# Performance work log

Measured on AMD Instinct MI355X. Metric: run time of the kernel, lower is better.

The kernel has to match this reference:

```python
import jax, jax.numpy as jnp
import numpy as np
import math

B, S, H, DK = 16, 4096, 16, 64
DM = H * DK          # 1024, d_model
QD = 1024            # q_d_model
KVD = 1024           # kv_d_model
MASK_P = 0.85        # randbool probability


def setup_inputs() -> dict:
    key = jax.random.key(0)
    ks = jax.random.split(key, 12)
    s = 0.02
    return {
        "q": jax.random.normal(ks[0], (B, 1, QD), jnp.float32),
        "k": jax.random.normal(ks[1], (B, S, KVD), jnp.float32),
        "v": jax.random.normal(ks[2], (B, S, KVD), jnp.float32),
        "Wq": jax.random.normal(ks[3], (QD, DM), jnp.float32) * s,
        "bq": jnp.zeros((DM,), jnp.float32),
        "Wk": jax.random.normal(ks[4], (KVD, DM), jnp.float32) * s,
        "bk": jnp.zeros((DM,), jnp.float32),
        "Wv": jax.random.normal(ks[5], (KVD, DM), jnp.float32) * s,
        "bv": jnp.zeros((DM,), jnp.float32),
        "Wo": jax.random.normal(ks[6], (DM, QD), jnp.float32) * s,
        "bo": jnp.zeros((QD,), jnp.float32),
        # randbool(shape, p=0.85): True where rand < p -> score zeroed
        "maskfill": jax.random.uniform(ks[7], (B, H, 1, S)) < MASK_P,
    }


def reference(q, k, v, Wq, bq, Wk, bk, Wv, bv, Wo, bo, maskfill):
    bs = q.shape[0]
    # projections -> [B, L, H, DK] -> [B, H, L, DK]
    qh = (q @ Wq + bq).reshape(bs, -1, H, DK).transpose(0, 2, 1, 3)  # [B,H,1,DK]
    kh = (k @ Wk + bk).reshape(bs, -1, H, DK).transpose(0, 2, 1, 3)  # [B,H,S,DK]
    vh = (v @ Wv + bv).reshape(bs, -1, H, DK).transpose(0, 2, 1, 3)  # [B,H,S,DK]

    scores1 = jnp.einsum("bhqd,bhkd->bhqk", qh, kh) / math.sqrt(DK)  # [B,H,1,S]

    # plain path (dropout = identity in eval)
    attn = jax.nn.softmax(scores1, axis=-1)
    out_h = jnp.einsum("bhqk,bhkd->bhqd", attn, vh)                  # [B,H,1,DK]

    # masked path: zero-fill (not -inf) masked raw scores, then softmax
    masked_scores = jnp.where(maskfill, 0.0, scores1)
    mattn = jax.nn.softmax(masked_scores, axis=-1)
    mout_h = jnp.einsum("bhqk,bhkd->bhqd", mattn, vh)

    concat = out_h.transpose(0, 2, 1, 3).reshape(bs, DM)
    mconcat = mout_h.transpose(0, 2, 1, 3).reshape(bs, DM)
    output = concat @ Wo + bo
    masked_output = mconcat @ Wo + bo
    return (output, masked_output)
```

## Files before the change

kernel.cpp:

```cpp
#include <hip/hip_runtime.h>
#include <stdint.h>

#define NB 16
#define NS 4096
#define NH 16
#define NC 1024

#define OFF_QHP   0u
#define OFF_QK    262144u
#define OFF_QB    524288u
#define OFF_SP    524608u
#define OFF_CTXP  532800u
#define OFF_CON   8921408u

__global__ __launch_bounds__(128) void k_qh(
    const float* __restrict__ q, const float* __restrict__ Wq, float* __restrict__ qhp)
{
    __shared__ float qs[64*16];
    int dz = blockIdx.x, cs = blockIdx.y;
    int tid = threadIdx.x;
    int d = dz*128 + tid;
#pragma unroll
    for (int j = 0; j < 2; ++j) {
        int idx = j*128 + tid;
        int b = idx >> 4, c4 = (idx & 15) << 2;
        float4 t = *(const float4*)(q + (size_t)b*NC + cs*64 + c4);
        qs[(c4+0)*16 + b] = t.x; qs[(c4+1)*16 + b] = t.y;
        qs[(c4+2)*16 + b] = t.z; qs[(c4+3)*16 + b] = t.w;
    }
    __syncthreads();
    float acc[16];
#pragma unroll
    for (int b = 0; b < 16; ++b) acc[b] = 0.f;
#pragma unroll 4
    for (int c = 0; c < 64; ++c) {
        float w = Wq[(size_t)(cs*64 + c)*NC + d];
        const float4* qr = (const float4*)(qs + c*16);
        float4 q0 = qr[0], q1 = qr[1], q2 = qr[2], q3 = qr[3];
        acc[0]  = fmaf(w, q0.x, acc[0]);  acc[1]  = fmaf(w, q0.y, acc[1]);
        acc[2]  = fmaf(w, q0.z, acc[2]);  acc[3]  = fmaf(w, q0.w, acc[3]);
        acc[4]  = fmaf(w, q1.x, acc[4]);  acc[5]  = fmaf(w, q1.y, acc[5]);
        acc[6]  = fmaf(w, q1.z, acc[6]);  acc[7]  = fmaf(w, q1.w, acc[7]);
        acc[8]  = fmaf(w, q2.x, acc[8]);  acc[9]  = fmaf(w, q2.y, acc[9]);
        acc[10] = fmaf(w, q2.z, acc[10]); acc[11] = fmaf(w, q2.w, acc[11]);
        acc[12] = fmaf(w, q3.x, acc[12]); acc[13] = fmaf(w, q3.y, acc[13]);
        acc[14] = fmaf(w, q3.z, acc[14]); acc[15] = fmaf(w, q3.w, acc[15]);
    }
#pragma unroll
    for (int b = 0; b < 16; ++b) qhp[((size_t)cs*16 + b)*NC + d] = acc[b];
}

__global__ __launch_bounds__(128) void k_qk(
    const float* __restrict__ qhp, const float* __restrict__ bq,
    const float* __restrict__ Wk, const float* __restrict__ bk,
    float* __restrict__ qko, float* __restrict__ qbv)
{
    int h = blockIdx.x;
    int c = blockIdx.y*128 + threadIdx.x;
    __shared__ float qs[16*64];
    for (int j = 0; j < 8; ++j) {
        int idx = j*128 + threadIdx.x;
        int b = idx >> 6, dd = idx & 63;
        float a = bq[h*64 + dd];
#pragma unroll
        for (int cs = 0; cs < 16; ++cs) a += qhp[((size_t)cs*16 + b)*NC + h*64 + dd];
        qs[idx] = a;
    }
    __syncthreads();
    const float* wr = Wk + (size_t)c*NC + h*64;
    float acc[16];
#pragma unroll
    for (int b = 0; b < 16; ++b) acc[b] = 0.f;
#pragma unroll 4
    for (int d = 0; d < 64; ++d) {
        float w = wr[d];
#pragma unroll
        for (int b = 0; b < 16; ++b) acc[b] = fmaf(qs[b*64 + d], w, acc[b]);
    }
#pragma unroll
    for (int b = 0; b < 16; ++b) qko[((size_t)b*NH + h)*NC + c] = acc[b];
    if (blockIdx.y == 0 && threadIdx.x < 16) {
        int b = threadIdx.x; float a = 0.f;
        for (int d = 0; d < 64; ++d) a = fmaf(qs[b*64 + d], bk[h*64 + d], a);
        qbv[b*NH + h] = a;
    }
}

#define QTS 20
#define SCOMP(BUF, W)                                                          \
    _Pragma("unroll")                                                          \
    for (int j = 0; j < 4; ++j) {                                              \
        const float* qp = qt + ((W)*16 + ph*4 + j)*QTS + hg*4;                 \
        float4 qv = *(const float4*)qp;                                        \
        _Pragma("unroll")                                                      \
        for (int i = 0; i < 4; ++i) {                                          \
            float kc = (j == 0) ? BUF[i].x : (j == 1) ? BUF[i].y               \
                     : (j == 2) ? BUF[i].z : BUF[i].w;                         \
            acc[i][0] = fmaf(kc, qv.x, acc[i][0]);                             \
            acc[i][1] = fmaf(kc, qv.y, acc[i][1]);                             \
            acc[i][2] = fmaf(kc, qv.z, acc[i][2]);                             \
            acc[i][3] = fmaf(kc, qv.w, acc[i][3]);                             \
        }                                                                      \
    }
__global__ __launch_bounds__(1024) void k_att(
    const float* __restrict__ kk, const float* __restrict__ vv,
    const float* __restrict__ qkm, const float* __restrict__ qbv,
    const void* __restrict__ mask, float* __restrict__ ctxp, float* __restrict__ Sp)
{
    __shared__ float qt[512*QTS];
    __shared__ float attl[256*32];
    __shared__ float red[16][2][16];
    int sb = blockIdx.x, b = blockIdx.y;
    int tid = threadIdx.x;
    int ph = tid & 3, hg = (tid >> 2) & 3, rg = tid >> 4;
    int srow = sb*256 + rg*4;

    int fl;
    {
        const uint4* mw = (const uint4*)mask;
        unsigned f = 0u, g = 0u;
#pragma unroll
        for (int j = 0; j < 8; ++j) {
            uint4 m4 = mw[j];
            f |= (m4.x == 0x3F800000u) | (m4.y == 0x3F800000u)
               | (m4.z == 0x3F800000u) | (m4.w == 0x3F800000u);
            g |= ((m4.x > 1u) & (m4.x != 0x3F800000u))
               | ((m4.y > 1u) & (m4.y != 0x3F800000u))
               | ((m4.z > 1u) & (m4.z != 0x3F800000u))
               | ((m4.w > 1u) & (m4.w != 0x3F800000u));
        }
        fl = f ? 2 : (g ? 1 : 0);
    }

    const float* kr = kk + ((size_t)b*NS + srow)*NC + ph*4;
    float acc[4][4];
#pragma unroll
    for (int i = 0; i < 4; ++i)
#pragma unroll
        for (int j = 0; j < 4; ++j) acc[i][j] = 0.f;

    for (int cz = 0; cz < 2; ++cz) {
        __syncthreads();
#pragma unroll
        for (int j = 0; j < 8; ++j) {
            int idx = j*1024 + tid;
            int h = idx >> 9, c = idx & 511;
            qt[c*QTS + h] = qkm[((size_t)b*NH + h)*NC + cz*512 + c];
        }
        __syncthreads();
        const float* kc0 = kr + cz*512;
        float4 A[4], B[4], T[4];
#pragma unroll
        for (int i = 0; i < 4; ++i) A[i] = *(const float4*)(kc0 + i*NC);
#pragma unroll
        for (int i = 0; i < 4; ++i) B[i] = *(const float4*)(kc0 + i*NC + 16);
        for (int w = 0; w < 32; w += 2) {
            if (w + 2 < 32) {
#pragma unroll
                for (int i = 0; i < 4; ++i)
                    T[i] = *(const float4*)(kc0 + i*NC + (w+2)*16);
            }
            SCOMP(A, w);
            if (w + 3 < 32) {
#pragma unroll
                for (int i = 0; i < 4; ++i)
                    A[i] = *(const float4*)(kc0 + i*NC + (w+3)*16);
            }
            SCOMP(B, (w+1));
#pragma unroll
            for (int i = 0; i < 4; ++i) { B[i] = A[i]; A[i] = T[i]; }
        }
    }
#pragma unroll
    for (int i = 0; i < 4; ++i)
#pragma unroll
        for (int j = 0; j < 4; ++j) {
            acc[i][j] += __shfl_xor(acc[i][j], 1, 64);
            acc[i][j] += __shfl_xor(acc[i][j], 2, 64);
        }
    float d0[4];
    if (ph == 0) {
#pragma unroll
        for (int j = 0; j < 4; ++j) d0[j] = acc[0][j];
    } else if (ph == 1) {
#pragma unroll
        for (int j = 0; j < 4; ++j) d0[j] = acc[1][j];
    } else if (ph == 2) {
#pragma unroll
        for (int j = 0; j < 4; ++j) d0[j] = acc[2][j];
    } else {
#pragma unroll
        for (int j = 0; j < 4; ++j) d0[j] = acc[3][j];
    }
    int lA = rg*4 + ph;
    int sA = sb*256 + lA;
    unsigned mA = 0;
    if (fl == 1) {
        const uint8_t* mp = (const uint8_t*)mask + (size_t)(b*NH + hg*4)*NS;
#pragma unroll
        for (int j = 0; j < 4; ++j)
            if (mp[(size_t)j*NS + sA]) mA |= (1u << j);
    } else if (fl == 2) {
        const float* mp = (const float*)mask + (size_t)(b*NH + hg*4)*NS;
#pragma unroll
        for (int j = 0; j < 4; ++j)
            if (mp[(size_t)j*NS + sA] != 0.f) mA |= (1u << j);
    } else {
        const int* mp = (const int*)mask + (size_t)(b*NH + hg*4)*NS;
#pragma unroll
        for (int j = 0; j < 4; ++j)
            if (mp[(size_t)j*NS + sA]) mA |= (1u << j);
    }
    float p0a[4], p1a[4], r0[4], r1[4];
#pragma unroll
    for (int j = 0; j < 4; ++j) {
        float qb = qbv[b*NH + hg*4 + j];
        float va = (d0[j] + qb) * 0.125f;
        p0a[j] = __expf(va);
        p1a[j] = (mA >> j & 1u) ? 1.0f : p0a[j];
        r0[j] = p0a[j];
        r1[j] = p1a[j];
    }
    {
        int swA = (lA & 7) << 2;
        *(float4*)(attl + lA*32 + ((hg*4) ^ swA))      = make_float4(p0a[0], p0a[1], p0a[2], p0a[3]);
        *(float4*)(attl + lA*32 + ((16 + hg*4) ^ swA)) = make_float4(p1a[0], p1a[1], p1a[2], p1a[3]);
    }
#pragma unroll
    for (int j = 0; j < 4; ++j) {
        r0[j] += __shfl_xor(r0[j], 1, 64);  r1[j] += __shfl_xor(r1[j], 1, 64);
        r0[j] += __shfl_xor(r0[j], 2, 64);  r1[j] += __shfl_xor(r1[j], 2, 64);
        r0[j] += __shfl_xor(r0[j], 16, 64); r1[j] += __shfl_xor(r1[j], 16, 64);
        r0[j] += __shfl_xor(r0[j], 32, 64); r1[j] += __shfl_xor(r1[j], 32, 64);
    }
    int wv = tid >> 6;
    if ((tid & 51) == 0) {
#pragma unroll
        for (int j = 0; j < 4; ++j) {
            red[wv][0][hg*4 + j] = r0[j];
            red[wv][1][hg*4 + j] = r1[j];
        }
    }
    __syncthreads();
    if (tid < 32) {
        int pa = tid >> 4, h = tid & 15;
        float a = 0.f;
#pragma unroll
        for (int w16 = 0; w16 < 16; ++w16) a += red[w16][pa][h];
        Sp[((size_t)b*16 + sb)*32 + tid] = a;
    }

    int cq = tid & 255, grp = tid >> 8;
    int p = grp >> 1, hh = grp & 1;
    float cacc[8][4];
#pragma unroll
    for (int u = 0; u < 8; ++u)
#pragma unroll
        for (int j = 0; j < 4; ++j) cacc[u][j] = 0.f;
    const float* vb = vv + ((size_t)b*NS + sb*256)*NC + cq*4;
    float4 vr[8], vn[8];
#pragma unroll
    for (int i = 0; i < 8; ++i) vr[i] = *(const float4*)(vb + (size_t)i*NC);
    int G0 = p*4 + hh*2;
    for (int r0q = 0; r0q < 256; r0q += 8) {
        if (r0q + 8 < 256) {
#pragma unroll
            for (int i = 0; i < 8; ++i)
                vn[i] = *(const float4*)(vb + (size_t)(r0q + 8 + i)*NC);
        }
#pragma unroll
        for (int i = 0; i < 8; ++i) {
            int r = r0q + i;
            const float* ar = attl + r*32;
            int lw = r & 7;
            float4 vcur = vr[i];
#pragma unroll
            for (int g2 = 0; g2 < 2; ++g2) {
                float4 aw = *(const float4*)(ar + (((G0 + g2) ^ lw) << 2));
                cacc[g2*4+0][0] = fmaf(aw.x, vcur.x, cacc[g2*4+0][0]);
                cacc[g2*4+0][1] = fmaf(aw.x, vcur.y, cacc[g2*4+0][1]);
                cacc[g2*4+0][2] = fmaf(aw.x, vcur.z, cacc[g2*4+0][2]);
                cacc[g2*4+0][3] = fmaf(aw.x, vcur.w, cacc[g2*4+0][3]);
                cacc[g2*4+1][0] = fmaf(aw.y, vcur.x, cacc[g2*4+1][0]);
                cacc[g2*4+1][1] = fmaf(aw.y, vcur.y, cacc[g2*4+1][1]);
                cacc[g2*4+1][2] = fmaf(aw.y, vcur.z, cacc[g2*4+1][2]);
                cacc[g2*4+1][3] = fmaf(aw.y, vcur.w, cacc[g2*4+1][3]);
                cacc[g2*4+2][0] = fmaf(aw.z, vcur.x, cacc[g2*4+2][0]);
                cacc[g2*4+2][1] = fmaf(aw.z, vcur.y, cacc[g2*4+2][1]);
                cacc[g2*4+2][2] = fmaf(aw.z, vcur.z, cacc[g2*4+2][2]);
                cacc[g2*4+2][3] = fmaf(aw.z, vcur.w, cacc[g2*4+2][3]);
                cacc[g2*4+3][0] = fmaf(aw.w, vcur.x, cacc[g2*4+3][0]);
                cacc[g2*4+3][1] = fmaf(aw.w, vcur.y, cacc[g2*4+3][1]);
                cacc[g2*4+3][2] = fmaf(aw.w, vcur.z, cacc[g2*4+3][2]);
                cacc[g2*4+3][3] = fmaf(aw.w, vcur.w, cacc[g2*4+3][3]);
            }
        }
#pragma unroll
        for (int i = 0; i < 8; ++i) vr[i] = vn[i];
    }
#pragma unroll
    for (int gh = 0; gh < 8; ++gh) {
        int head = hh*8 + gh;
        *(float4*)(ctxp + ((((size_t)sb*2 + p)*NB + b)*NH + head)*NC + cq*4)
            = make_float4(cacc[gh][0], cacc[gh][1], cacc[gh][2], cacc[gh][3]);
    }
}

__global__ __launch_bounds__(256) void k_outhN(
    const float* __restrict__ ctxp, const float* __restrict__ Sp,
    const float* __restrict__ Wv, const float* __restrict__ bv,
    float* __restrict__ con)
{
    int b = blockIdx.y, p = blockIdx.z;
    int dx = blockIdx.x;
    int d = dx*256 + threadIdx.x;
    int h0 = dx*4;
    __shared__ float cl[4*NC];
    float Sinv[4];
#pragma unroll
    for (int j = 0; j < 4; ++j) {
        float a = 0.f;
        for (int sb = 0; sb < 16; ++sb)
            a += Sp[((size_t)b*16 + sb)*32 + p*16 + h0 + j];
        Sinv[j] = 1.f / a;
    }
#pragma unroll
    for (int hh = 0; hh < 4; ++hh) {
        for (int cc = threadIdx.x; cc < NC; cc += 256) {
            float a = 0.f;
#pragma unroll
            for (int ss = 0; ss < 16; ++ss)
                a += ctxp[((((size_t)ss*2 + p)*NB + b)*NH + h0 + hh)*NC + cc];
            cl[hh*NC + cc] = a * Sinv[hh];
        }
    }
    __syncthreads();
    const float* c2 = cl + ((threadIdx.x >> 6) << 10);
    float a0=0.f,a1=0.f,a2=0.f,a3=0.f;
    for (int c = 0; c < NC; c += 4) {
        a0 = fmaf(c2[c+0], Wv[(size_t)(c+0)*NC + d], a0);
        a1 = fmaf(c2[c+1], Wv[(size_t)(c+1)*NC + d], a1);
        a2 = fmaf(c2[c+2], Wv[(size_t)(c+2)*NC + d], a2);
        a3 = fmaf(c2[c+3], Wv[(size_t)(c+3)*NC + d], a3);
    }
    con[((size_t)p*NB + b)*NC + d] = (a0+a1)+(a2+a3) + bv[d];
}

__global__ __launch_bounds__(256) void k_out(
    const float* __restrict__ con, const float* __restrict__ Wo,
    const float* __restrict__ bo, float* __restrict__ out)
{
    int b = blockIdx.y, p = blockIdx.z;
    int o = blockIdx.x*256 + threadIdx.x;
    __shared__ float cl[NC];
    for (int i = threadIdx.x; i < NC; i += 256)
        cl[i] = con[((size_t)p*NB + b)*NC + i];
    __syncthreads();
    float a0=0.f,a1=0.f,a2=0.f,a3=0.f;
    for (int m = 0; m < NC; m += 4) {
        a0 = fmaf(cl[m+0], Wo[(size_t)(m+0)*NC + o], a0);
        a1 = fmaf(cl[m+1], Wo[(size_t)(m+1)*NC + o], a1);
        a2 = fmaf(cl[m+2], Wo[(size_t)(m+2)*NC + o], a2);
        a3 = fmaf(cl[m+3], Wo[(size_t)(m+3)*NC + o], a3);
    }
    out[(size_t)p*NB*NC + (size_t)b*NC + o] = (a0+a1)+(a2+a3) + bo[o];
}

extern "C" void kernel_launch(void* const* d_in, const int* in_sizes, int n_in,
                              void* d_out, int out_size, void* d_ws, size_t ws_size,
                              hipStream_t stream)
{
    (void)in_sizes; (void)n_in; (void)out_size; (void)ws_size;
    const float* q  = (const float*)d_in[0];
    const float* k  = (const float*)d_in[1];
    const float* v  = (const float*)d_in[2];
    const float* Wq = (const float*)d_in[3];
    const float* bq = (const float*)d_in[4];
    const float* Wk = (const float*)d_in[5];
    const float* bk = (const float*)d_in[6];
    const float* Wv = (const float*)d_in[7];
    const float* bv = (const float*)d_in[8];
    const float* Wo = (const float*)d_in[9];
    const float* bo = (const float*)d_in[10];
    const void*  mk = d_in[11];

    float* ws   = (float*)d_ws;
    float* qhp  = ws + OFF_QHP;
    float* qkv  = ws + OFF_QK;
    float* qbv  = ws + OFF_QB;
    float* Sp   = ws + OFF_SP;
    float* ctxp = ws + OFF_CTXP;
    float* con  = ws + OFF_CON;
    float* out  = (float*)d_out;

    k_qh<<<dim3(8, 16), 128, 0, stream>>>(q, Wq, qhp);
    k_qk<<<dim3(16, 8), 128, 0, stream>>>(qhp, bq, Wk, bk, qkv, qbv);
    k_att<<<dim3(16, 16), 1024, 0, stream>>>(k, v, qkv, qbv, mk, ctxp, Sp);
    k_outhN<<<dim3(4, NB, 2), 256, 0, stream>>>(ctxp, Sp, Wv, bv, con);
    k_out<<<dim3(4, NB, 2), 256, 0, stream>>>(con, Wo, bo, out);
}
```

Measured before the change: 305.2 us.

## Split fused attention kernel into separate scores and context kernels

```diff
diff --git a/kernel.cpp b/kernel.cpp
--- a/kernel.cpp
+++ b/kernel.cpp
@@ -9,9 +9,10 @@
 #define OFF_QHP   0u
 #define OFF_QK    262144u
 #define OFF_QB    524288u
-#define OFF_SP    524608u
-#define OFF_CTXP  532800u
-#define OFF_CON   8921408u
+#define OFF_SP    524544u
+#define OFF_ATT   540928u
+#define OFF_CTXP  2638080u
+#define OFF_CON   11026688u
 
 __global__ __launch_bounds__(128) void k_qh(
     const float* __restrict__ q, const float* __restrict__ Wq, float* __restrict__ qhp)
@@ -87,7 +88,7 @@
 }
 
 #define QTS 20
-#define SCOMP(BUF, W)                                                          \
+#define SCOMP4(BUF, W)                                                         \
     _Pragma("unroll")                                                          \
     for (int j = 0; j < 4; ++j) {                                              \
         const float* qp = qt + ((W)*16 + ph*4 + j)*QTS + hg*4;                 \
@@ -102,18 +103,17 @@
             acc[i][3] = fmaf(kc, qv.w, acc[i][3]);                             \
         }                                                                      \
     }
-__global__ __launch_bounds__(1024) void k_att(
-    const float* __restrict__ kk, const float* __restrict__ vv,
-    const float* __restrict__ qkm, const float* __restrict__ qbv,
-    const void* __restrict__ mask, float* __restrict__ ctxp, float* __restrict__ Sp)
-{
-    __shared__ float qt[512*QTS];
-    __shared__ float attl[256*32];
-    __shared__ float red[16][2][16];
+__global__ __launch_bounds__(512, 4) void k_scoresS(
+    const float* __restrict__ kk, const float* __restrict__ qkm,
+    const float* __restrict__ qbv, const void* __restrict__ mask,
+    float* __restrict__ att, float* __restrict__ Sp)
+{
+    __shared__ float qt[256*QTS];
+    __shared__ float red[8][2][16];
     int sb = blockIdx.x, b = blockIdx.y;
     int tid = threadIdx.x;
     int ph = tid & 3, hg = (tid >> 2) & 3, rg = tid >> 4;
-    int srow = sb*256 + rg*4;
+    int srow = sb*128 + rg*4;
 
     int fl;
     {
@@ -139,36 +139,28 @@
 #pragma unroll
         for (int j = 0; j < 4; ++j) acc[i][j] = 0.f;
 
-    for (int cz = 0; cz < 2; ++cz) {
+    for (int cz = 0; cz < 4; ++cz) {
         __syncthreads();
 #pragma unroll
         for (int j = 0; j < 8; ++j) {
-            int idx = j*1024 + tid;
-            int h = idx >> 9, c = idx & 511;
-            qt[c*QTS + h] = qkm[((size_t)b*NH + h)*NC + cz*512 + c];
+            int idx = j*512 + tid;
+            int h = idx >> 8, c = idx & 255;
+            qt[c*QTS + h] = qkm[((size_t)b*NH + h)*NC + cz*256 + c];
         }
         __syncthreads();
-        const float* kc0 = kr + cz*512;
-        float4 A[4], B[4], T[4];
+        const float* kc0 = kr + cz*256;
+        float4 A[4], B[4];
 #pragma unroll
         for (int i = 0; i < 4; ++i) A[i] = *(const float4*)(kc0 + i*NC);
-#pragma unroll
-        for (int i = 0; i < 4; ++i) B[i] = *(const float4*)(kc0 + i*NC + 16);
-        for (int w = 0; w < 32; w += 2) {
-            if (w + 2 < 32) {
+        for (int w = 0; w < 16; ++w) {
+            if (w < 15) {
 #pragma unroll
                 for (int i = 0; i < 4; ++i)
-                    T[i] = *(const float4*)(kc0 + i*NC + (w+2)*16);
+                    B[i] = *(const float4*)(kc0 + i*NC + (w+1)*16);
             }
-            SCOMP(A, w);
-            if (w + 3 < 32) {
-#pragma unroll
-                for (int i = 0; i < 4; ++i)
-                    A[i] = *(const float4*)(kc0 + i*NC + (w+3)*16);
-            }
-            SCOMP(B, (w+1));
-#pragma unroll
-            for (int i = 0; i < 4; ++i) { B[i] = A[i]; A[i] = T[i]; }
+            SCOMP4(A, w);
+#pragma unroll
+            for (int i = 0; i < 4; ++i) A[i] = B[i];
         }
     }
 #pragma unroll
@@ -193,7 +185,7 @@
         for (int j = 0; j < 4; ++j) d0[j] = acc[3][j];
     }
     int lA = rg*4 + ph;
-    int sA = sb*256 + lA;
+    int sA = sb*128 + lA;
     unsigned mA = 0;
     if (fl == 1) {
         const uint8_t* mp = (const uint8_t*)mask + (size_t)(b*NH + hg*4)*NS;
@@ -222,9 +214,9 @@
         r1[j] = p1a[j];
     }
     {
-        int swA = (lA & 7) << 2;
-        *(float4*)(attl + lA*32 + ((hg*4) ^ swA))      = make_float4(p0a[0], p0a[1], p0a[2], p0a[3]);
-        *(float4*)(attl + lA*32 + ((16 + hg*4) ^ swA)) = make_float4(p1a[0], p1a[1], p1a[2], p1a[3]);
+        float* arow = att + ((size_t)b*NS + sA)*32;
+        *(float4*)(arow + hg*4)      = make_float4(p0a[0], p0a[1], p0a[2], p0a[3]);
+        *(float4*)(arow + 16 + hg*4) = make_float4(p1a[0], p1a[1], p1a[2], p1a[3]);
     }
 #pragma unroll
     for (int j = 0; j < 4; ++j) {
@@ -246,62 +238,67 @@
         int pa = tid >> 4, h = tid & 15;
         float a = 0.f;
 #pragma unroll
-        for (int w16 = 0; w16 < 16; ++w16) a += red[w16][pa][h];
-        Sp[((size_t)b*16 + sb)*32 + tid] = a;
-    }
-
-    int cq = tid & 255, grp = tid >> 8;
-    int p = grp >> 1, hh = grp & 1;
+        for (int w8 = 0; w8 < 8; ++w8) a += red[w8][pa][h];
+        Sp[((size_t)b*32 + sb)*32 + tid] = a;
+    }
+}
+
+__global__ __launch_bounds__(512, 4) void k_ctxS(
+    const float* __restrict__ vv, const float* __restrict__ att,
+    float* __restrict__ ctxp)
+{
+    __shared__ float atl[256*32];
+    int ss = blockIdx.x, b = blockIdx.y, cz = blockIdx.z;
+    int tid = threadIdx.x;
+    int cq = tid & 127, pg = tid >> 7;
+    {
+        const float4* src = (const float4*)(att + ((size_t)b*NS + ss*256)*32);
+#pragma unroll
+        for (int j = 0; j < 4; ++j)
+            ((float4*)atl)[j*512 + tid] = src[j*512 + tid];
+    }
+    __syncthreads();
     float cacc[8][4];
 #pragma unroll
     for (int u = 0; u < 8; ++u)
 #pragma unroll
         for (int j = 0; j < 4; ++j) cacc[u][j] = 0.f;
-    const float* vb = vv + ((size_t)b*NS + sb*256)*NC + cq*4;
-    float4 vr[8], vn[8];
-#pragma unroll
-    for (int i = 0; i < 8; ++i) vr[i] = *(const float4*)(vb + (size_t)i*NC);
-    int G0 = p*4 + hh*2;
-    for (int r0q = 0; r0q < 256; r0q += 8) {
-        if (r0q + 8 < 256) {
-#pragma unroll
-            for (int i = 0; i < 8; ++i)
-                vn[i] = *(const float4*)(vb + (size_t)(r0q + 8 + i)*NC);
-        }
-#pragma unroll
-        for (int i = 0; i < 8; ++i) {
-            int r = r0q + i;
-            const float* ar = attl + r*32;
-            int lw = r & 7;
-            float4 vcur = vr[i];
-#pragma unroll
-            for (int g2 = 0; g2 < 2; ++g2) {
-                float4 aw = *(const float4*)(ar + (((G0 + g2) ^ lw) << 2));
-                cacc[g2*4+0][0] = fmaf(aw.x, vcur.x, cacc[g2*4+0][0]);
-                cacc[g2*4+0][1] = fmaf(aw.x, vcur.y, cacc[g2*4+0][1]);
-                cacc[g2*4+0][2] = fmaf(aw.x, vcur.z, cacc[g2*4+0][2]);
-                cacc[g2*4+0][3] = fmaf(aw.x, vcur.w, cacc[g2*4+0][3]);
-                cacc[g2*4+1][0] = fmaf(aw.y, vcur.x, cacc[g2*4+1][0]);
-                cacc[g2*4+1][1] = fmaf(aw.y, vcur.y, cacc[g2*4+1][1]);
-                cacc[g2*4+1][2] = fmaf(aw.y, vcur.z, cacc[g2*4+1][2]);
-                cacc[g2*4+1][3] = fmaf(aw.y, vcur.w, cacc[g2*4+1][3]);
-                cacc[g2*4+2][0] = fmaf(aw.z, vcur.x, cacc[g2*4+2][0]);
-                cacc[g2*4+2][1] = fmaf(aw.z, vcur.y, cacc[g2*4+2][1]);
-                cacc[g2*4+2][2] = fmaf(aw.z, vcur.z, cacc[g2*4+2][2]);
-                cacc[g2*4+2][3] = fmaf(aw.z, vcur.w, cacc[g2*4+2][3]);
-                cacc[g2*4+3][0] = fmaf(aw.w, vcur.x, cacc[g2*4+3][0]);
-                cacc[g2*4+3][1] = fmaf(aw.w, vcur.y, cacc[g2*4+3][1]);
-                cacc[g2*4+3][2] = fmaf(aw.w, vcur.z, cacc[g2*4+3][2]);
-                cacc[g2*4+3][3] = fmaf(aw.w, vcur.w, cacc[g2*4+3][3]);
-            }
-        }
-#pragma unroll
-        for (int i = 0; i < 8; ++i) vr[i] = vn[i];
+    const float* vb = vv + ((size_t)b*NS + ss*256)*NC + cz*512 + cq*4;
+    float4 vcur = *(const float4*)vb;
+    for (int r = 0; r < 256; ++r) {
+        float4 vnxt;
+        if (r < 255) vnxt = *(const float4*)(vb + (size_t)(r+1)*NC);
+        const float* ar = atl + r*32 + pg*8;
+        float4 a0 = *(const float4*)(ar);
+        float4 a1 = *(const float4*)(ar + 4);
+#pragma unroll
+        for (int g2 = 0; g2 < 2; ++g2) {
+            float4 aw = (g2 == 0) ? a0 : a1;
+            cacc[g2*4+0][0] = fmaf(aw.x, vcur.x, cacc[g2*4+0][0]);
+            cacc[g2*4+0][1] = fmaf(aw.x, vcur.y, cacc[g2*4+0][1]);
+            cacc[g2*4+0][2] = fmaf(aw.x, vcur.z, cacc[g2*4+0][2]);
+            cacc[g2*4+0][3] = fmaf(aw.x, vcur.w, cacc[g2*4+0][3]);
+            cacc[g2*4+1][0] = fmaf(aw.y, vcur.x, cacc[g2*4+1][0]);
+            cacc[g2*4+1][1] = fmaf(aw.y, vcur.y, cacc[g2*4+1][1]);
+            cacc[g2*4+1][2] = fmaf(aw.y, vcur.z, cacc[g2*4+1][2]);
+            cacc[g2*4+1][3] = fmaf(aw.y, vcur.w, cacc[g2*4+1][3]);
+            cacc[g2*4+2][0] = fmaf(aw.z, vcur.x, cacc[g2*4+2][0]);
+            cacc[g2*4+2][1] = fmaf(aw.z, vcur.y, cacc[g2*4+2][1]);
+            cacc[g2*4+2][2] = fmaf(aw.z, vcur.z, cacc[g2*4+2][2]);
+            cacc[g2*4+2][3] = fmaf(aw.z, vcur.w, cacc[g2*4+2][3]);
+            cacc[g2*4+3][0] = fmaf(aw.w, vcur.x, cacc[g2*4+3][0]);
+            cacc[g2*4+3][1] = fmaf(aw.w, vcur.y, cacc[g2*4+3][1]);
+            cacc[g2*4+3][2] = fmaf(aw.w, vcur.z, cacc[g2*4+3][2]);
+            cacc[g2*4+3][3] = fmaf(aw.w, vcur.w, cacc[g2*4+3][3]);
+        }
+        vcur = vnxt;
+        if ((r & 7) == 7) __syncthreads();
     }
 #pragma unroll
     for (int gh = 0; gh < 8; ++gh) {
-        int head = hh*8 + gh;
-        *(float4*)(ctxp + ((((size_t)sb*2 + p)*NB + b)*NH + head)*NC + cq*4)
+        int G = pg*8 + gh;
+        int p = G >> 4, h = G & 15;
+        *(float4*)(ctxp + ((((size_t)ss*2 + p)*NB + b)*NH + h)*NC + cz*512 + cq*4)
             = make_float4(cacc[gh][0], cacc[gh][1], cacc[gh][2], cacc[gh][3]);
     }
 }
@@ -320,8 +317,8 @@
 #pragma unroll
     for (int j = 0; j < 4; ++j) {
         float a = 0.f;
-        for (int sb = 0; sb < 16; ++sb)
-            a += Sp[((size_t)b*16 + sb)*32 + p*16 + h0 + j];
+        for (int sb = 0; sb < 32; ++sb)
+            a += Sp[((size_t)b*32 + sb)*32 + p*16 + h0 + j];
         Sinv[j] = 1.f / a;
     }
 #pragma unroll
@@ -389,13 +386,15 @@
     float* qkv  = ws + OFF_QK;
     float* qbv  = ws + OFF_QB;
     float* Sp   = ws + OFF_SP;
+    float* att  = ws + OFF_ATT;
     float* ctxp = ws + OFF_CTXP;
     float* con  = ws + OFF_CON;
     float* out  = (float*)d_out;
 
     k_qh<<<dim3(8, 16), 128, 0, stream>>>(q, Wq, qhp);
     k_qk<<<dim3(16, 8), 128, 0, stream>>>(qhp, bq, Wk, bk, qkv, qbv);
-    k_att<<<dim3(16, 16), 1024, 0, stream>>>(k, v, qkv, qbv, mk, ctxp, Sp);
+    k_scoresS<<<dim3(32, 16), 512, 0, stream>>>(k, qkv, qbv, mk, att, Sp);
+    k_ctxS<<<dim3(16, 16, 2), 512, 0, stream>>>(v, att, ctxp);
     k_outhN<<<dim3(4, NB, 2), 256, 0, stream>>>(ctxp, Sp, Wv, bv, con);
     k_out<<<dim3(4, NB, 2), 256, 0, stream>>>(con, Wo, bo, out);
 }
```

New measurement: 279.9 us. 1.09x faster.
